# Performance work log

Hardware: AMD Instinct MI355X
Metric: run time of the kernel (lower is better)

Reference implementation:

```python
import jax, jax.numpy as jnp
import numpy as np

N = 100_000
E = 1_600_000
IN_DIM = 21
HID = 256
OUT = 256


def setup_inputs() -> dict:
    key = jax.random.key(0)
    ks = jax.random.split(key, 10)
    node_scalar = jax.random.normal(ks[0], (N, IN_DIM), dtype=jnp.float32)
    edge_index = jax.random.randint(ks[1], (2, E), 0, N, dtype=jnp.int64)
    s_in = 1.0 / np.sqrt(IN_DIM)
    s_h = 1.0 / np.sqrt(HID)
    W_in = jax.random.uniform(ks[2], (IN_DIM, HID), jnp.float32, -s_in, s_in)
    b_in = jax.random.uniform(ks[3], (HID,), jnp.float32, -s_in, s_in)
    W_self = jax.random.uniform(ks[4], (HID, HID), jnp.float32, -s_h, s_h)
    b_self = jax.random.uniform(ks[5], (HID,), jnp.float32, -s_h, s_h)
    W_nei = jax.random.uniform(ks[6], (HID, HID), jnp.float32, -s_h, s_h)
    b_nei = jax.random.uniform(ks[7], (HID,), jnp.float32, -s_h, s_h)
    W_out = jax.random.uniform(ks[8], (HID, OUT), jnp.float32, -s_h, s_h)
    b_out = jax.random.uniform(ks[9], (OUT,), jnp.float32, -s_h, s_h)
    return {
        "node_scalar": node_scalar,
        "W_in": W_in, "b_in": b_in,
        "W_self": W_self, "b_self": b_self,
        "W_nei": W_nei, "b_nei": b_nei,
        "W_out": W_out, "b_out": b_out,
        "edge_index": edge_index,
    }


def reference(node_scalar, W_in, b_in, W_self, b_self, W_nei, b_nei, W_out, b_out, edge_index):
    # x = relu(Linear(node_scalar)); dropout is identity in eval mode
    x = jax.nn.relu(node_scalar @ W_in + b_in)           # (N, H)
    n = x.shape[0]
    src, dst = edge_index[0], edge_index[1]
    msg = x[src]                                          # (E, H) gather
    agg = jax.ops.segment_sum(msg, dst, num_segments=n)   # (N, H) scatter-add
    deg = jax.ops.segment_sum(jnp.ones((dst.shape[0],), dtype=x.dtype), dst, num_segments=n)
    agg = agg / jnp.maximum(deg, 1.0)[:, None]            # degree mean (clamp_min 1)
    h = jax.nn.relu(x @ W_self + b_self + agg @ W_nei + b_nei)
    g = h.mean(axis=0)                                    # global mean pool -> (H,)
    return g @ W_out + b_out                              # (OUT,)
```

## Files before the change

### kernel.cpp

```cpp
#include <hip/hip_runtime.h>
#include <hip/hip_bf16.h>

#define HID 256
#define IND 21
#define PB 6400
#define MAXB 512

typedef short short8 __attribute__((ext_vector_type(8)));
typedef float floatx16 __attribute__((ext_vector_type(16)));
typedef float floatx2 __attribute__((ext_vector_type(2)));

__device__ inline unsigned short f2bf(float f) {
  __hip_bfloat16 h = __float2bfloat16(f);
  union { __hip_bfloat16 h; unsigned short u; } c;
  c.h = h;
  return c.u;
}

__device__ inline unsigned int pk_bf16_trunc(floatx2 p) {
  union { float f; unsigned int u; } a, b;
  a.f = p.x; b.f = p.y;
  return (b.u & 0xffff0000u) | (a.u >> 16);
}

__device__ inline void acc8p(uint2 v, floatx2* a) {
  a[0] += __builtin_amdgcn_cvt_pk_f32_fp8((int)v.x, false);
  a[1] += __builtin_amdgcn_cvt_pk_f32_fp8((int)v.x, true);
  a[2] += __builtin_amdgcn_cvt_pk_f32_fp8((int)v.y, false);
  a[3] += __builtin_amdgcn_cvt_pk_f32_fp8((int)v.y, true);
}

__device__ inline short8 mk_s8(unsigned a, unsigned b, unsigned c, unsigned d) {
  union { uint4 u; short8 s; } x; x.u = make_uint4(a, b, c, d); return x.s;
}

__device__ inline short8 dec8(uint2 v) {
  unsigned w0 = pk_bf16_trunc(__builtin_amdgcn_cvt_pk_f32_fp8((int)v.x, false));
  unsigned w1 = pk_bf16_trunc(__builtin_amdgcn_cvt_pk_f32_fp8((int)v.x, true));
  unsigned w2 = pk_bf16_trunc(__builtin_amdgcn_cvt_pk_f32_fp8((int)v.y, false));
  unsigned w3 = pk_bf16_trunc(__builtin_amdgcn_cvt_pk_f32_fp8((int)v.y, true));
  return mk_s8(w0, w1, w2, w3);
}

__global__ __launch_bounds__(256) void k_front(
    const float* __restrict__ ns, const float* __restrict__ Win,
    const float* __restrict__ bin, uint2* __restrict__ xq2,
    uint2* __restrict__ Aqx,
    const float* __restrict__ Wself, const float* __restrict__ Wnei,
    unsigned short* __restrict__ Bf16,
    const int* __restrict__ dst, int* __restrict__ bcnt,
    int N, int E, int nb2, int G1) {
  int blk = blockIdx.x;
  int tid = threadIdx.x;
  if (blk < G1) {
    __shared__ __align__(16) float s[8][24];
    __shared__ float fx[8][257];
    int nb = blk * 8;
    if (tid < 8 * IND) {
      int idx = nb * IND + tid;
      s[tid / IND][tid % IND] = (idx < N * IND) ? ns[idx] : 0.f;
    }
    float w[IND];
#pragma unroll
    for (int k = 0; k < IND; k++) w[k] = Win[k * HID + tid];
    float b = bin[tid];
    __syncthreads();
#pragma unroll
    for (int j = 0; j < 8; j++) {
      float acc = b;
      const float4* sp = (const float4*)&s[j][0];
#pragma unroll
      for (int k4 = 0; k4 < 5; k4++) {
        float4 t = sp[k4];
        acc += t.x * w[k4 * 4] + t.y * w[k4 * 4 + 1] +
               t.z * w[k4 * 4 + 2] + t.w * w[k4 * 4 + 3];
      }
      acc += s[j][20] * w[20];
      fx[j][tid] = acc > 0.f ? acc : 0.f;
    }
    __syncthreads();
    {
      int j = tid & 7, u = tid >> 3;
      int node = nb + j;
      if (node < N) {
        const float* fp = &fx[j][u * 8];
        int lo0 = __builtin_amdgcn_cvt_pk_fp8_f32(fp[0], fp[1], 0, false);
        int w0  = __builtin_amdgcn_cvt_pk_fp8_f32(fp[2], fp[3], lo0, true);
        int lo1 = __builtin_amdgcn_cvt_pk_fp8_f32(fp[4], fp[5], 0, false);
        int w1  = __builtin_amdgcn_cvt_pk_fp8_f32(fp[6], fp[7], lo1, true);
        uint2 val = make_uint2((unsigned)w0, (unsigned)w1);
        xq2[(size_t)node * 32 + u] = val;
        int g = node >> 5, row = node & 31, c = u >> 1, hi = u & 1;
        Aqx[(size_t)(g * 16 + c) * 64 + hi * 32 + row] = val;
      }
    }
  } else if (blk < G1 + 256) {
    int n = blk - G1;
    int ct = n >> 5, l5 = n & 31;
#pragma unroll
    for (int t = 0; t < 2; t++) {
      int k = tid + t * 256;
      float v = (k < HID) ? Wself[k * HID + n] : Wnei[(k - HID) * HID + n];
      int c = k >> 4, kin = k & 15;
      int lane = (kin >> 3) * 32 + l5;
      int j = kin & 7;
      Bf16[(size_t)((c * 8 + ct) * 64 + lane) * 8 + j] = f2bf(v);
    }
  } else {
    __shared__ int lh[MAXB];
    int e0 = (blk - G1 - 256) * PB;
    for (int b = tid; b < nb2; b += 256) lh[b] = 0;
    __syncthreads();
    int c = min(PB, E - e0);
    for (int i = tid; i < c; i += 256) atomicAdd(&lh[dst[e0 + i] >> 8], 1);
    __syncthreads();
    for (int b = tid; b < nb2; b += 256)
      if (lh[b]) atomicAdd(&bcnt[b], lh[b]);
  }
}

__global__ __launch_bounds__(512) void k_bscan(
    const int* __restrict__ bcnt, int* __restrict__ bbase, int* __restrict__ bcur,
    int* __restrict__ row_start, int E, int N, int nb2) {
  __shared__ int ts[512];
  int tid = threadIdx.x;
  int v = (tid < nb2) ? bcnt[tid] : 0;
  ts[tid] = v;
  __syncthreads();
  for (int off = 1; off < 512; off <<= 1) {
    int t = (tid >= off) ? ts[tid - off] : 0;
    __syncthreads();
    ts[tid] += t;
    __syncthreads();
  }
  if (tid < nb2) { bbase[tid] = ts[tid] - v; bcur[tid] = ts[tid] - v; }
  if (tid == 0) { bbase[nb2] = E; row_start[N] = E; }
}

__global__ __launch_bounds__(256) void k_part(
    const int* __restrict__ src, const int* __restrict__ dst,
    int* __restrict__ bcur, unsigned int* __restrict__ ebuf, int E, int nb2) {
  __shared__ int lh[MAXB];
  int tid = threadIdx.x;
  int e0 = blockIdx.x * PB;
  for (int b = tid; b < nb2; b += 256) lh[b] = 0;
  __syncthreads();
  int cnt = min(PB, E - e0);
  for (int i = tid; i < cnt; i += 256) atomicAdd(&lh[dst[e0 + i] >> 8], 1);
  __syncthreads();
  for (int b = tid; b < nb2; b += 256) {
    int c = lh[b];
    lh[b] = (c > 0) ? atomicAdd(&bcur[b], c) : 0;
  }
  __syncthreads();
  for (int i = tid; i < cnt; i += 256) {
    int s = src[e0 + i];
    int d = dst[e0 + i];
    int pos = atomicAdd(&lh[d >> 8], 1);
    ebuf[pos] = ((unsigned)s << 8) | ((unsigned)d & 255u);
  }
}

__global__ __launch_bounds__(256) void k_fill2(
    const unsigned int* __restrict__ ebuf, const int* __restrict__ bbase,
    int* __restrict__ row_start, unsigned int* __restrict__ csr, int N) {
  __shared__ int lcnt[256];
  __shared__ int lcur[256];
  __shared__ int ts[256];
  int b = blockIdx.x;
  int tid = threadIdx.x;
  int start = bbase[b], end = bbase[b + 1];
  lcnt[tid] = 0;
  __syncthreads();
  for (int i = start + tid; i < end; i += 256)
    atomicAdd(&lcnt[ebuf[i] & 255u], 1);
  __syncthreads();
  int v = lcnt[tid];
  ts[tid] = v;
  __syncthreads();
  for (int off = 1; off < 256; off <<= 1) {
    int t = (tid >= off) ? ts[tid - off] : 0;
    __syncthreads();
    ts[tid] += t;
    __syncthreads();
  }
  int excl = start + ts[tid] - v;
  int node = (b << 8) + tid;
  if (node < N) row_start[node] = excl;
  lcur[tid] = excl;
  __syncthreads();
  for (int i = start + tid; i < end; i += 256) {
    unsigned int e = ebuf[i];
    int pos = atomicAdd(&lcur[e & 255u], 1);
    csr[pos] = e & ~255u;
  }
}

__global__ __launch_bounds__(256) void k_agg(
    const unsigned char* __restrict__ xqb, const unsigned int* __restrict__ csrb,
    const int* __restrict__ row_start, uint2* __restrict__ Aqagg, int N, int n0) {
  __shared__ uint2 ld[8][33];
  int tid = threadIdx.x;
  int lane = tid & 63;
  int w = tid >> 6;
  int half = lane >> 5;
  int l32 = lane & 31;
  unsigned lo = (unsigned)(l32 * 8);

  int nl = w * 2 + half;
  int wid = n0 + blockIdx.x * 8 + nl;
  int cw = (wid < N) ? wid : (N - 1);
  int start = row_start[cw];
  int end = row_start[cw + 1];
  int c = end - start;
  floatx2 a[4], b[4], d[4], e[4];
#pragma unroll
  for (int j = 0; j < 4; j++) {
    a[j] = (floatx2){0.f, 0.f}; b[j] = (floatx2){0.f, 0.f};
    d[j] = (floatx2){0.f, 0.f}; e[j] = (floatx2){0.f, 0.f};
  }
  int i = 0;
  while (i < c) {
    int nb = min(32, c - i);
    int sel = (l32 < nb) ? l32 : 0;
    unsigned idx = csrb[start + i + sel];
    int j = 0;
    for (; j + 8 <= nb; j += 8) {
      unsigned o0 = (unsigned)__shfl((int)idx, j + 0, 32) + lo;
      unsigned o1 = (unsigned)__shfl((int)idx, j + 1, 32) + lo;
      unsigned o2 = (unsigned)__shfl((int)idx, j + 2, 32) + lo;
      unsigned o3 = (unsigned)__shfl((int)idx, j + 3, 32) + lo;
      unsigned o4 = (unsigned)__shfl((int)idx, j + 4, 32) + lo;
      unsigned o5 = (unsigned)__shfl((int)idx, j + 5, 32) + lo;
      unsigned o6 = (unsigned)__shfl((int)idx, j + 6, 32) + lo;
      unsigned o7 = (unsigned)__shfl((int)idx, j + 7, 32) + lo;
      uint2 v0 = *(const uint2*)(xqb + o0);
      uint2 v1 = *(const uint2*)(xqb + o1);
      uint2 v2 = *(const uint2*)(xqb + o2);
      uint2 v3 = *(const uint2*)(xqb + o3);
      uint2 v4 = *(const uint2*)(xqb + o4);
      uint2 v5 = *(const uint2*)(xqb + o5);
      uint2 v6 = *(const uint2*)(xqb + o6);
      uint2 v7 = *(const uint2*)(xqb + o7);
      acc8p(v0, a); acc8p(v1, b); acc8p(v2, d); acc8p(v3, e);
      acc8p(v4, a); acc8p(v5, b); acc8p(v6, d); acc8p(v7, e);
    }
    for (; j + 4 <= nb; j += 4) {
      unsigned o0 = (unsigned)__shfl((int)idx, j + 0, 32) + lo;
      unsigned o1 = (unsigned)__shfl((int)idx, j + 1, 32) + lo;
      unsigned o2 = (unsigned)__shfl((int)idx, j + 2, 32) + lo;
      unsigned o3 = (unsigned)__shfl((int)idx, j + 3, 32) + lo;
      uint2 v0 = *(const uint2*)(xqb + o0);
      uint2 v1 = *(const uint2*)(xqb + o1);
      uint2 v2 = *(const uint2*)(xqb + o2);
      uint2 v3 = *(const uint2*)(xqb + o3);
      acc8p(v0, a); acc8p(v1, b); acc8p(v2, d); acc8p(v3, e);
    }
    for (; j < nb; j++) {
      unsigned o0 = (unsigned)__shfl((int)idx, j, 32) + lo;
      uint2 v0 = *(const uint2*)(xqb + o0);
      acc8p(v0, a);
    }
    i += nb;
  }
#pragma unroll
  for (int j = 0; j < 4; j++) a[j] += b[j] + d[j] + e[j];

  float inv = 1.0f / fmaxf((float)c, 1.0f);
  float f[8];
#pragma unroll
  for (int j = 0; j < 4; j++) {
    f[2 * j] = a[j].x * inv;
    f[2 * j + 1] = a[j].y * inv;
  }
  int lo0 = __builtin_amdgcn_cvt_pk_fp8_f32(f[0], f[1], 0, false);
  int w0  = __builtin_amdgcn_cvt_pk_fp8_f32(f[2], f[3], lo0, true);
  int lo1 = __builtin_amdgcn_cvt_pk_fp8_f32(f[4], f[5], 0, false);
  int w1  = __builtin_amdgcn_cvt_pk_fp8_f32(f[6], f[7], lo1, true);
  ld[nl][l32] = make_uint2((unsigned)w0, (unsigned)w1);
  __syncthreads();

  int g = (n0 >> 5) + (blockIdx.x >> 2);
  int r0 = (blockIdx.x & 3) * 8;
  int s = tid >> 3, j = tid & 7;
  Aqagg[(size_t)g * 1024 + (size_t)s * 32 + r0 + j] = ld[j][s];
}

__global__ __launch_bounds__(256, 3) void k_h(
    const unsigned char* __restrict__ Aqx, const unsigned char* __restrict__ Aqagg,
    const unsigned char* __restrict__ Bf8, const float* __restrict__ bself,
    const float* __restrict__ bnei, float* __restrict__ gsum, int N, int nfull) {
  __shared__ float colsum[128];
  int bid = blockIdx.x;
  int bx, by;
  if (bid < nfull) {
    bx = (bid >> 4) * 8 + (bid & 7);
    by = (bid >> 3) & 1;
  } else {
    int rem = bid - nfull;
    bx = (nfull >> 1) + (rem >> 1);
    by = rem & 1;
  }
  int tid = threadIdx.x;
  int lane = tid & 63;
  int w = tid >> 6;
  int wr = w >> 1, wc = w & 1;
  int l32 = lane & 31, half = lane >> 5;
  int rowBase = bx * 128;

  if (tid < 128) colsum[tid] = 0.f;

  floatx16 acc[2][2];
#pragma unroll
  for (int i = 0; i < 2; i++)
#pragma unroll
    for (int j = 0; j < 2; j++) acc[i][j] = (floatx16)(0.f);

  size_t agrp = (size_t)(bx * 4 + wr * 2) * 8192 + (size_t)(lane * 8);
  size_t bgrp = ((size_t)(by * 4 + wc * 2) * 64 + lane) * 16;

  for (int ch = 0; ch < 8; ch++) {
    const unsigned char* Aq = (ch < 4) ? Aqx : Aqagg;
    const unsigned char* abase = Aq + agrp + (size_t)(ch & 3) * 2048;
#pragma unroll
    for (int cl = 0; cl < 4; cl++) {
      uint2 a0 = *(const uint2*)(abase + cl * 512);
      uint2 a1 = *(const uint2*)(abase + 8192 + cl * 512);
      const unsigned char* bbase = Bf8 + bgrp + (size_t)(ch * 4 + cl) * 8192;
      short8 b0 = *(const short8*)(bbase);
      short8 b1 = *(const short8*)(bbase + 1024);
      short8 af0 = dec8(a0);
      short8 af1 = dec8(a1);
      acc[0][0] = __builtin_amdgcn_mfma_f32_32x32x16_bf16(af0, b0, acc[0][0], 0, 0, 0);
      acc[1][0] = __builtin_amdgcn_mfma_f32_32x32x16_bf16(af1, b0, acc[1][0], 0, 0, 0);
      acc[0][1] = __builtin_amdgcn_mfma_f32_32x32x16_bf16(af0, b1, acc[0][1], 0, 0, 0);
      acc[1][1] = __builtin_amdgcn_mfma_f32_32x32x16_bf16(af1, b1, acc[1][1], 0, 0, 0);
    }
  }

  __syncthreads();
#pragma unroll
  for (int ctw = 0; ctw < 2; ctw++) {
    int lcol = (wc * 2 + ctw) * 32 + l32;
    int gcol = by * 128 + lcol;
    float bb = bself[gcol] + bnei[gcol];
    float psum = 0.f;
#pragma unroll
    for (int rt = 0; rt < 2; rt++) {
#pragma unroll
      for (int r = 0; r < 16; r++) {
        int rw = rowBase + wr * 64 + rt * 32 + (r & 3) + 8 * (r >> 2) + 4 * half;
        float v = acc[rt][ctw][r] + bb;
        v = v > 0.f ? v : 0.f;
        if (rw < N) psum += v;
      }
    }
    atomicAdd(&colsum[lcol], psum);
  }
  __syncthreads();
  if (tid < 128) atomicAdd(&gsum[by * 128 + tid], colsum[tid]);
}

__global__ __launch_bounds__(HID) void k_out(
    const float* __restrict__ gsum, const float* __restrict__ Wout,
    const float* __restrict__ bout, float* __restrict__ out, float invN) {
  __shared__ float g[HID];
  int c = threadIdx.x;
  g[c] = gsum[c] * invN;
  __syncthreads();
  float acc = bout[c];
#pragma unroll 8
  for (int k = 0; k < HID; k++) acc += g[k] * Wout[k * HID + c];
  out[c] = acc;
}

extern "C" void kernel_launch(void* const* d_in, const int* in_sizes, int n_in,
                              void* d_out, int out_size, void* d_ws, size_t ws_size,
                              hipStream_t stream) {
  const float* ns    = (const float*)d_in[0];
  const float* Win   = (const float*)d_in[1];
  const float* bin   = (const float*)d_in[2];
  const float* Wself = (const float*)d_in[3];
  const float* bself = (const float*)d_in[4];
  const float* Wnei  = (const float*)d_in[5];
  const float* bnei  = (const float*)d_in[6];
  const float* Wout  = (const float*)d_in[7];
  const float* bout  = (const float*)d_in[8];
  const int*   eidx  = (const int*)d_in[9];

  int N = in_sizes[0] / IND;
  int E = in_sizes[9] / 2;
  const int* src = eidx;
  const int* dst = eidx + E;
  int nb2 = (N + 255) >> 8;
  int nbx = (N + 127) / 128;
  size_t NGU = (size_t)nbx * 4 * 16 * 64;

  unsigned int* xq     = (unsigned int*)d_ws;
  uint2* Aqx           = (uint2*)(xq + (size_t)N * 64);
  uint2* Aqagg         = Aqx + NGU;
  unsigned short* Bf16 = (unsigned short*)(Aqagg + NGU);
  unsigned int* csr  = (unsigned int*)(Bf16 + 256 * 512);
  unsigned int* ebuf = csr + E;
  int* row_start = (int*)(ebuf + E);
  int* bcnt      = row_start + N + 1;
  float* gsum    = (float*)(bcnt + MAXB);
  int* bbase     = (int*)(gsum + HID);
  int* bcur      = bbase + MAXB + 1;

  hipMemsetAsync(bcnt, 0, (MAXB + HID) * sizeof(int), stream);

  int G1 = (N + 7) / 8;
  int pgrid = (E + PB - 1) / PB;
  k_front<<<G1 + 256 + pgrid, 256, 0, stream>>>(
      ns, Win, bin, (uint2*)xq, Aqx, Wself, Wnei, Bf16, dst, bcnt,
      N, E, nb2, G1);

  k_bscan<<<1, 512, 0, stream>>>(bcnt, bbase, bcur, row_start, E, N, nb2);
  k_part<<<pgrid, 256, 0, stream>>>(src, dst, bcur, ebuf, E, nb2);
  k_fill2<<<nb2, 256, 0, stream>>>(ebuf, bbase, row_start, csr, N);

  int H = (((N / 2) + 31) / 32) * 32;
  if (H > N) H = N;
  int agrid1 = H / 8;
  int agrid2 = (N - H + 7) / 8;
  if (agrid1 > 0)
    k_agg<<<agrid1, 256, 0, stream>>>((const unsigned char*)xq, csr, row_start,
                                      Aqagg, N, 0);
  if (agrid2 > 0)
    k_agg<<<agrid2, 256, 0, stream>>>((const unsigned char*)xq, csr, row_start,
                                      Aqagg, N, H);

  int nblocks = nbx * 2;
  int nfull = (nblocks / 16) * 16;
  k_h<<<nblocks, 256, 0, stream>>>((const unsigned char*)Aqx,
                                   (const unsigned char*)Aqagg,
                                   (const unsigned char*)Bf16,
                                   bself, bnei, gsum, N, nfull);

  k_out<<<1, HID, 0, stream>>>(gsum, Wout, bout, (float*)d_out, 1.0f / (float)N);
}
```

Before: 287.5 us.

## Shrink k_h row tile to 64, stage A via LDS double-buffer, merge agg launches

The k_h GEMM tile drops from 128 to 64 rows per block, and each wave now computes a 32x64 output instead of 64x64, which halves the accumulators and raises the occupancy hint to 4. The fp8 A operand is prefetched into a double-buffered LDS tile with global_load_lds, one k-chunk ahead of the MFMAs. The two split k_agg launches become one. In exchange, each block reads B for only half as many rows, so B traffic per row doubles, and a barrier is added every chunk.

```diff
diff --git a/kernel.cpp b/kernel.cpp
--- a/kernel.cpp
+++ b/kernel.cpp
@@ -40,6 +40,12 @@
   unsigned w2 = pk_bf16_trunc(__builtin_amdgcn_cvt_pk_f32_fp8((int)v.y, false));
   unsigned w3 = pk_bf16_trunc(__builtin_amdgcn_cvt_pk_f32_fp8((int)v.y, true));
   return mk_s8(w0, w1, w2, w3);
+}
+
+__device__ inline void gl16(const unsigned char* g, unsigned char* l) {
+  __builtin_amdgcn_global_load_lds(
+      (const __attribute__((address_space(1))) unsigned char*)g,
+      (__attribute__((address_space(3))) unsigned char*)l, 16, 0, 0);
 }
 
 __global__ __launch_bounds__(256) void k_front(
@@ -198,7 +204,7 @@
 
 __global__ __launch_bounds__(256) void k_agg(
     const unsigned char* __restrict__ xqb, const unsigned int* __restrict__ csrb,
-    const int* __restrict__ row_start, uint2* __restrict__ Aqagg, int N, int n0) {
+    const int* __restrict__ row_start, uint2* __restrict__ Aqagg, int N) {
   __shared__ uint2 ld[8][33];
   int tid = threadIdx.x;
   int lane = tid & 63;
@@ -208,7 +214,7 @@
   unsigned lo = (unsigned)(l32 * 8);
 
   int nl = w * 2 + half;
-  int wid = n0 + blockIdx.x * 8 + nl;
+  int wid = blockIdx.x * 8 + nl;
   int cw = (wid < N) ? wid : (N - 1);
   int start = row_start[cw];
   int end = row_start[cw + 1];
@@ -280,16 +286,17 @@
   ld[nl][l32] = make_uint2((unsigned)w0, (unsigned)w1);
   __syncthreads();
 
-  int g = (n0 >> 5) + (blockIdx.x >> 2);
+  int g = blockIdx.x >> 2;
   int r0 = (blockIdx.x & 3) * 8;
   int s = tid >> 3, j = tid & 7;
   Aqagg[(size_t)g * 1024 + (size_t)s * 32 + r0 + j] = ld[j][s];
 }
 
-__global__ __launch_bounds__(256, 3) void k_h(
+__global__ __launch_bounds__(256, 4) void k_h(
     const unsigned char* __restrict__ Aqx, const unsigned char* __restrict__ Aqagg,
     const unsigned char* __restrict__ Bf8, const float* __restrict__ bself,
     const float* __restrict__ bnei, float* __restrict__ gsum, int N, int nfull) {
+  __shared__ __align__(16) unsigned char As[2][4096];
   __shared__ float colsum[128];
   int bid = blockIdx.x;
   int bx, by;
@@ -306,54 +313,54 @@
   int w = tid >> 6;
   int wr = w >> 1, wc = w & 1;
   int l32 = lane & 31, half = lane >> 5;
-  int rowBase = bx * 128;
+  int rowBase = bx * 64;
 
   if (tid < 128) colsum[tid] = 0.f;
 
-  floatx16 acc[2][2];
-#pragma unroll
-  for (int i = 0; i < 2; i++)
-#pragma unroll
-    for (int j = 0; j < 2; j++) acc[i][j] = (floatx16)(0.f);
-
-  size_t agrp = (size_t)(bx * 4 + wr * 2) * 8192 + (size_t)(lane * 8);
+  floatx16 acc[2];
+  acc[0] = (floatx16)(0.f);
+  acc[1] = (floatx16)(0.f);
+
+  size_t a_src = (size_t)(bx * 2 + wr) * 8192 + (size_t)(w & 1) * 1024 +
+                 (size_t)(lane * 16);
+  {
+    gl16(Aqx + a_src, As[0] + w * 1024);
+  }
+
   size_t bgrp = ((size_t)(by * 4 + wc * 2) * 64 + lane) * 16;
 
   for (int ch = 0; ch < 8; ch++) {
-    const unsigned char* Aq = (ch < 4) ? Aqx : Aqagg;
-    const unsigned char* abase = Aq + agrp + (size_t)(ch & 3) * 2048;
+    int buf = ch & 1;
+    __syncthreads();
+    if (ch < 7) {
+      int cn = ch + 1;
+      const unsigned char* Aq = (cn < 4) ? Aqx : Aqagg;
+      gl16(Aq + a_src + (size_t)(cn & 3) * 2048, As[buf ^ 1] + w * 1024);
+    }
 #pragma unroll
     for (int cl = 0; cl < 4; cl++) {
-      uint2 a0 = *(const uint2*)(abase + cl * 512);
-      uint2 a1 = *(const uint2*)(abase + 8192 + cl * 512);
+      uint2 av = *(const uint2*)&As[buf][wr * 2048 + cl * 512 + lane * 8];
+      short8 afr = dec8(av);
       const unsigned char* bbase = Bf8 + bgrp + (size_t)(ch * 4 + cl) * 8192;
       short8 b0 = *(const short8*)(bbase);
       short8 b1 = *(const short8*)(bbase + 1024);
-      short8 af0 = dec8(a0);
-      short8 af1 = dec8(a1);
-      acc[0][0] = __builtin_amdgcn_mfma_f32_32x32x16_bf16(af0, b0, acc[0][0], 0, 0, 0);
-      acc[1][0] = __builtin_amdgcn_mfma_f32_32x32x16_bf16(af1, b0, acc[1][0], 0, 0, 0);
-      acc[0][1] = __builtin_amdgcn_mfma_f32_32x32x16_bf16(af0, b1, acc[0][1], 0, 0, 0);
-      acc[1][1] = __builtin_amdgcn_mfma_f32_32x32x16_bf16(af1, b1, acc[1][1], 0, 0, 0);
-    }
-  }
-
-  __syncthreads();
+      acc[0] = __builtin_amdgcn_mfma_f32_32x32x16_bf16(afr, b0, acc[0], 0, 0, 0);
+      acc[1] = __builtin_amdgcn_mfma_f32_32x32x16_bf16(afr, b1, acc[1], 0, 0, 0);
+    }
+  }
+
 #pragma unroll
   for (int ctw = 0; ctw < 2; ctw++) {
-    int lcol = (wc * 2 + ctw) * 32 + l32;
+    int lcol = wc * 64 + ctw * 32 + l32;
     int gcol = by * 128 + lcol;
     float bb = bself[gcol] + bnei[gcol];
     float psum = 0.f;
 #pragma unroll
-    for (int rt = 0; rt < 2; rt++) {
-#pragma unroll
-      for (int r = 0; r < 16; r++) {
-        int rw = rowBase + wr * 64 + rt * 32 + (r & 3) + 8 * (r >> 2) + 4 * half;
-        float v = acc[rt][ctw][r] + bb;
-        v = v > 0.f ? v : 0.f;
-        if (rw < N) psum += v;
-      }
+    for (int r = 0; r < 16; r++) {
+      int rw = rowBase + wr * 32 + (r & 3) + 8 * (r >> 2) + 4 * half;
+      float v = acc[ctw][r] + bb;
+      v = v > 0.f ? v : 0.f;
+      if (rw < N) psum += v;
     }
     atomicAdd(&colsum[lcol], psum);
   }
@@ -420,18 +427,12 @@
   k_part<<<pgrid, 256, 0, stream>>>(src, dst, bcur, ebuf, E, nb2);
   k_fill2<<<nb2, 256, 0, stream>>>(ebuf, bbase, row_start, csr, N);
 
-  int H = (((N / 2) + 31) / 32) * 32;
-  if (H > N) H = N;
-  int agrid1 = H / 8;
-  int agrid2 = (N - H + 7) / 8;
-  if (agrid1 > 0)
-    k_agg<<<agrid1, 256, 0, stream>>>((const unsigned char*)xq, csr, row_start,
-                                      Aqagg, N, 0);
-  if (agrid2 > 0)
-    k_agg<<<agrid2, 256, 0, stream>>>((const unsigned char*)xq, csr, row_start,
-                                      Aqagg, N, H);
-
-  int nblocks = nbx * 2;
+  int agrid = (N + 7) / 8;
+  k_agg<<<agrid, 256, 0, stream>>>((const unsigned char*)xq, csr, row_start,
+                                   Aqagg, N);
+
+  int nbx64 = (N + 63) / 64;
+  int nblocks = nbx64 * 2;
   int nfull = (nblocks / 16) * 16;
   k_h<<<nblocks, 256, 0, stream>>>((const unsigned char*)Aqx,
                                    (const unsigned char*)Aqagg,
```

Result: slower. 308.6 us (+7.4%).
